# Performance work log

Measured on AMD Instinct MI355X. Metric: run time of the kernel, lower is better.

Reference implementation:

```python
import jax, jax.numpy as jnp
import numpy as np

B, T, C = 2, 2048, 1024
N_HEAD = 16
HEAD_DIM = C // N_HEAD
N_WORLDS = 4


def setup_inputs() -> dict:
    key = jax.random.key(0)
    kx, kq, kk, kv, kp, ka = jax.random.split(key, 6)
    scale = 0.02
    x = jax.random.normal(kx, (B, T, C), dtype=jnp.float32)
    Wq = jax.random.normal(kq, (C, C), dtype=jnp.float32) * scale
    Wk = jax.random.normal(kk, (C, C), dtype=jnp.float32) * scale
    Wv = jax.random.normal(kv, (C, C), dtype=jnp.float32) * scale
    Wproj = jax.random.normal(kp, (C, C), dtype=jnp.float32) * scale
    acc = jax.random.randint(ka, (N_WORLDS, N_WORLDS), 0, 2, dtype=jnp.int32)
    # ensure every world accesses itself so no softmax row is fully masked
    acc = acc.at[jnp.arange(N_WORLDS), jnp.arange(N_WORLDS)].set(1)
    return {"x": x, "Wq": Wq, "Wk": Wk, "Wv": Wv, "Wproj": Wproj,
            "accessibility": acc}


def reference(x, Wq, Wk, Wv, Wproj, accessibility):
    Bd, Td, Cd = x.shape
    # torch Linear: y = x @ W.T  -> project then split heads
    q = (x @ Wq.T).reshape(Bd, Td, N_HEAD, HEAD_DIM).transpose(0, 2, 1, 3)
    k = (x @ Wk.T).reshape(Bd, Td, N_HEAD, HEAD_DIM).transpose(0, 2, 1, 3)
    v = (x @ Wv.T).reshape(Bd, Td, N_HEAD, HEAD_DIM).transpose(0, 2, 1, 3)

    scores = jnp.einsum('bhqd,bhkd->bhqk', q, k) / jnp.sqrt(
        jnp.asarray(HEAD_DIM, dtype=x.dtype))

    # Kripke modal mask: token t lives in world t % n_worlds (necessity: \u25a1)
    world = jnp.arange(Td) % accessibility.shape[0]
    modal_mask = accessibility[world][:, world]          # (T, T) 0/1
    scores = jnp.where(modal_mask[None, None] == 0, -jnp.inf, scores)

    attn = jax.nn.softmax(scores, axis=-1)
    out = jnp.einsum('bhqk,bhkd->bhqd', attn, v)
    out = out.transpose(0, 2, 1, 3).reshape(Bd, Td, Cd)
    return out @ Wproj.T
```

## Files before the change

### kernel.cpp

```cpp
#include <hip/hip_runtime.h>
#include <hip/hip_bf16.h>
#include <stdint.h>


typedef __attribute__((ext_vector_type(8))) __bf16   bf16x8;
typedef __attribute__((ext_vector_type(4))) float    f32x4;
typedef __attribute__((ext_vector_type(8))) ushort   ushort8;

__device__ __forceinline__ ushort f2bf(float x) {
    uint32_t u = __float_as_uint(x);
    return (ushort)((u + 0x7fffu + ((u >> 16) & 1u)) >> 16);
}
__device__ __forceinline__ float sentinel(float v, float s) {
    return (fabsf(v) < 1e30f) ? v : s;
}
__device__ __forceinline__ f32x4 mfma16(bf16x8 a, bf16x8 b, f32x4 c) {
    return __builtin_amdgcn_mfma_f32_16x16x32_bf16(a, b, c, 0, 0, 0);
}
__device__ __forceinline__ ushort2 pk2(float a, float b) {
    __hip_bfloat162 h = __float22bfloat162_rn(make_float2(a, b));
    union { __hip_bfloat162 h; ushort2 u; } c; c.h = h; return c.u;
}
__device__ __forceinline__ ushort4 cvt4(float4 v) {
    ushort2 lo = pk2(v.x, v.y), hi = pk2(v.z, v.w);
    ushort4 r; r.x = lo.x; r.y = lo.y; r.z = hi.x; r.w = hi.y; return r;
}
__device__ __forceinline__ ushort4 cvt4s(float4 v, float s) {
    ushort2 lo = pk2(v.x * s, v.y * s), hi = pk2(v.z * s, v.w * s);
    ushort4 r; r.x = lo.x; r.y = lo.y; r.z = hi.x; r.w = hi.y; return r;
}
__device__ __forceinline__ float fexp2(float x) {
#if __has_builtin(__builtin_amdgcn_exp2f)
    return __builtin_amdgcn_exp2f(x);
#else
    return exp2f(x);
#endif
}
__device__ __forceinline__ void gld16(const ushort* g, ushort* l) {
    auto* g1 = reinterpret_cast<const __attribute__((address_space(1))) uint32_t*>(
        reinterpret_cast<uintptr_t>(g));
    auto* l3 = reinterpret_cast<__attribute__((address_space(3))) uint32_t*>(
        reinterpret_cast<uintptr_t>(l));
    __builtin_amdgcn_global_load_lds(g1, l3, 16, 0, 0);
}

__device__ __forceinline__ int swz(int row, int ch) {
    return row * 64 + ((ch ^ (row & 7)) * 8);
}

__device__ __forceinline__ int wperm(int ts) {
    return ((ts & 3) << 9) | (ts >> 2);
}

__device__ __forceinline__ int vshuf(int r) {
    return ((r & 31) << 2) | (r >> 5);
}

#define QSCALE 0.1803368801111244f

__global__ __launch_bounds__(256) void cvt_prepass(
        const float* __restrict__ x,  const float* __restrict__ Wq,
        const float* __restrict__ Wk, const float* __restrict__ Wv,
        const float* __restrict__ Wp,
        ushort* __restrict__ xb,  ushort* __restrict__ wqb,
        ushort* __restrict__ wkb, ushort* __restrict__ wvb,
        ushort* __restrict__ wpb)
{
    int gid = blockIdx.x;
    const float* src; ushort* dst; float sc = 1.0f; int boff;
    if (gid < 4096)      { src = x;  dst = xb;  boff = gid; }
    else if (gid < 5120) { src = Wq; dst = wqb; boff = gid - 4096; sc = QSCALE; }
    else if (gid < 6144) { src = Wk; dst = wkb; boff = gid - 5120; }
    else if (gid < 7168) { src = Wv; dst = wvb; boff = gid - 6144; }
    else                 { src = Wp; dst = wpb; boff = gid - 7168; }
    size_t idx = (size_t)boff * 1024 + threadIdx.x * 4;
    float4 v = *(const float4*)&src[idx];
    *(ushort4*)&dst[idx] = cvt4s(v, sc);
}

__global__ __launch_bounds__(256) void gemm_qkv_b(
        const ushort* __restrict__ xb,
        const ushort* __restrict__ wqb, const ushort* __restrict__ wkb,
        const ushort* __restrict__ wvb,
        ushort* __restrict__ Cq, ushort* __restrict__ Ck,
        ushort* __restrict__ Cv)
{
    __shared__ ushort As[128 * 64];
    __shared__ ushort Bs[128 * 64];

    const int lin  = blockIdx.x + 24 * blockIdx.y;
    const int xcd  = lin & 7;
    const int slot = lin >> 3;
    const int bx   = (xcd & 1) * 12 + (slot % 12);
    const int by   = (xcd >> 1) * 8 + (slot / 12);

    const int sel = bx >> 3;
    const ushort* __restrict__ Bw = sel == 0 ? wqb : (sel == 1 ? wkb : wvb);
    ushort* __restrict__ C        = sel == 0 ? Cq : (sel == 1 ? Ck : Cv);

    const int tid  = threadIdx.x;
    const int lane = tid & 63;
    const int wave = tid >> 6;
    const int quad = lane >> 4;
    const int l15  = lane & 15;
    const int tokb = by * 128;
    const int chb  = (bx & 7) * 128;
    const int wm = (wave & 1) * 64, wn = (wave >> 1) * 64;

    f32x4 acc[4][4] = {};

    for (int k0 = 0; k0 < 1024; k0 += 64) {
        __syncthreads();
        #pragma unroll
        for (int j = 0; j < 4; ++j) {
            int cb = j * 256 + wave * 64;
            int ci = cb + lane;
            int r  = ci >> 3;
            int qc = (ci & 7) ^ (r & 7);
            if (sel < 2) {
                gld16(&Bw[(size_t)(chb + r) * 1024 + k0 + qc * 8], &As[cb * 8]);
                gld16(&xb[(size_t)(tokb + r) * 1024 + k0 + qc * 8], &Bs[cb * 8]);
            } else {
                gld16(&xb[(size_t)(tokb + vshuf(r)) * 1024 + k0 + qc * 8], &As[cb * 8]);
                gld16(&Bw[(size_t)(chb + r) * 1024 + k0 + qc * 8], &Bs[cb * 8]);
            }
        }
        __syncthreads();

        bf16x8 af[2][4], bfr[2][4];
        #pragma unroll
        for (int f = 0; f < 2; ++f)
            #pragma unroll
            for (int i = 0; i < 4; ++i) {
                int ch = f * 4 + quad;
                af[f][i]  = *(const bf16x8*)&As[swz(wm + i * 16 + l15, ch)];
                bfr[f][i] = *(const bf16x8*)&Bs[swz(wn + i * 16 + l15, ch)];
            }
        #pragma unroll
        for (int f = 0; f < 2; ++f)
            #pragma unroll
            for (int i = 0; i < 4; ++i)
                #pragma unroll
                for (int t = 0; t < 4; ++t)
                    acc[i][t] = mfma16(af[f][i], bfr[f][t], acc[i][t]);
    }

    if (sel < 2) {
        #pragma unroll
        for (int i = 0; i < 4; ++i) {
            int ch = chb + wm + i * 16 + quad * 4;
            int hh = ch >> 6, d0 = ch & 63;
            #pragma unroll
            for (int t = 0; t < 4; ++t) {
                int n = tokb + wn + t * 16 + l15;
                int b = n >> 11, ts = n & 2047;
                ushort4 hv;
                hv.x = f2bf(sentinel(acc[i][t][0], 1e8f));
                hv.y = f2bf(sentinel(acc[i][t][1], 1e8f));
                hv.z = f2bf(sentinel(acc[i][t][2], 1e8f));
                hv.w = f2bf(sentinel(acc[i][t][3], 1e8f));
                *(ushort4*)&C[((size_t)((b << 4) | hh) * 2048 + wperm(ts)) * 64 + d0] = hv;
            }
        }
    } else {
        const int b = tokb >> 11;
        #pragma unroll
        for (int i = 0; i < 4; ++i) {
            int mi0 = wm + i * 16 + quad * 4;
            int colbase = ((mi0 >> 5) << 9) + ((tokb & 2047) >> 2) + (mi0 & 31);
            #pragma unroll
            for (int t = 0; t < 4; ++t) {
                int n = chb + wn + t * 16 + l15;
                int hh = n >> 6, d = n & 63;
                ushort4 hv;
                hv.x = f2bf(sentinel(acc[i][t][0], 1e8f));
                hv.y = f2bf(sentinel(acc[i][t][1], 1e8f));
                hv.z = f2bf(sentinel(acc[i][t][2], 1e8f));
                hv.w = f2bf(sentinel(acc[i][t][3], 1e8f));
                *(ushort4*)&C[((size_t)((b << 4) | hh) * 64 + d) * 2048 + colbase] = hv;
            }
        }
    }
}

__global__ __launch_bounds__(256) void gemm_proj_b(
        const ushort* __restrict__ O, const ushort* __restrict__ wpb,
        float* __restrict__ out)
{
    __shared__ ushort As[128 * 64];
    __shared__ ushort Bs[64 * 64];

    const int lin  = blockIdx.x + 16 * blockIdx.y;
    const int xcd  = lin & 7;
    const int slot = lin >> 3;
    const int bx   = (xcd & 1) * 8 + (slot % 8);
    const int by   = (xcd >> 1) * 8 + (slot / 8);

    const int tid  = threadIdx.x;
    const int lane = tid & 63;
    const int wave = tid >> 6;
    const int quad = lane >> 4;
    const int l15  = lane & 15;
    const int bm = by * 128, bn = bx * 64;
    const int wm = (wave & 1) * 64,  wn = (wave >> 1) * 32;

    f32x4 acc[4][2] = {};

    for (int k0 = 0; k0 < 1024; k0 += 64) {
        __syncthreads();
        int h = k0 >> 6;
        #pragma unroll
        for (int j = 0; j < 4; ++j) {
            int cb = j * 256 + wave * 64;
            int ci = cb + lane;
            int r  = ci >> 3;
            int qc = (ci & 7) ^ (r & 7);
            int m = bm + r;
            int b = m >> 11, ts = m & 2047;
            gld16(&O[((((size_t)(b * 16 + h)) * 2048 + wperm(ts)) << 6) + qc * 8],
                  &As[cb * 8]);
        }
        #pragma unroll
        for (int j = 0; j < 2; ++j) {
            int cb = j * 256 + wave * 64;
            int ci = cb + lane;
            int r  = ci >> 3;
            int qc = (ci & 7) ^ (r & 7);
            gld16(&wpb[(size_t)(bn + r) * 1024 + k0 + qc * 8], &Bs[cb * 8]);
        }
        __syncthreads();

        bf16x8 af[2][4], bfr[2][2];
        #pragma unroll
        for (int f = 0; f < 2; ++f) {
            int ch = f * 4 + quad;
            #pragma unroll
            for (int i = 0; i < 4; ++i)
                af[f][i] = *(const bf16x8*)&As[swz(wm + i * 16 + l15, ch)];
            #pragma unroll
            for (int t = 0; t < 2; ++t)
                bfr[f][t] = *(const bf16x8*)&Bs[swz(wn + t * 16 + l15, ch)];
        }
        #pragma unroll
        for (int f = 0; f < 2; ++f)
            #pragma unroll
            for (int i = 0; i < 4; ++i)
                #pragma unroll
                for (int t = 0; t < 2; ++t)
                    acc[i][t] = mfma16(af[f][i], bfr[f][t], acc[i][t]);
    }

    #pragma unroll
    for (int i = 0; i < 4; ++i)
        #pragma unroll
        for (int t = 0; t < 2; ++t)
            #pragma unroll
            for (int r = 0; r < 4; ++r) {
                int m = bm + wm + i * 16 + quad * 4 + r;
                int n = bn + wn + t * 16 + l15;
                out[(size_t)m * 1024 + n] = sentinel(acc[i][t][r], 100.0f);
            }
}

__global__ __launch_bounds__(256) void attn_kernel(
        ushort* __restrict__ Q, const ushort* __restrict__ Kk,
        const ushort* __restrict__ Vt_g, const int* __restrict__ accm)
{
    __shared__ ushort Ks[2][64 * 64];
    __shared__ ushort Vt[2][64 * 64];
    __shared__ ushort Ps[4][32 * 64];

    const int tid  = threadIdx.x;
    const int lane = tid & 63;
    const int wave = tid >> 6;
    const int quad = lane >> 4;
    const int l15  = lane & 15;
    const int bh = blockIdx.x, qt = blockIdx.y;

    ushort*       Qg = Q    + ((size_t)bh * 2048 + qt * 128) * 64;
    const ushort* Kg = Kk   + (size_t)bh * 2048 * 64;
    const ushort* Vg = Vt_g + (size_t)bh * 64 * 2048;

    const int qworld = qt >> 2;
    int gpack = 0, ng = 0;
    #pragma unroll
    for (int w = 0; w < 4; ++w)
        if (accm[qworld * 4 + w] != 0) { gpack |= w << (ng * 8); ++ng; }
    const int nkt = ng * 8;
    auto ktof = [&](int i) {
        return ((((gpack >> ((i >> 3) << 3)) & 3) << 3) | (i & 7));
    };

    bf16x8 aq[2][2];
    #pragma unroll
    for (int i = 0; i < 2; ++i)
        #pragma unroll
        for (int f = 0; f < 2; ++f)
            aq[i][f] = *(const bf16x8*)
                &Qg[(wave * 32 + i * 16 + l15) * 64 + f * 32 + quad * 8];

    bf16x8 aones;
    #pragma unroll
    for (int j = 0; j < 8; ++j) aones[j] = (__bf16)1.0f;

    f32x4 oacc[4][2] = {};
    f32x4 lacc[2] = {};

    auto stage = [&](int kt, int buf) {
        #pragma unroll
        for (int j = 0; j < 2; ++j) {
            int cb = j * 256 + wave * 64;
            int ci = cb + lane;
            int r  = ci >> 3;
            int qc = (ci & 7) ^ (r & 7);
            gld16(&Kg[((size_t)kt * 64 + r) * 64 + qc * 8], &Ks[buf][cb * 8]);
            gld16(&Vg[(size_t)r * 2048 + kt * 64 + qc * 8], &Vt[buf][cb * 8]);
        }
    };

    stage(ktof(0), 0);
    for (int it = 0; it < nkt; ++it) {
        const int cur = it & 1;
        __syncthreads();
        if (it < nkt - 1) stage(ktof(it + 1), cur ^ 1);

        f32x4 st[4][2] = {};
        #pragma unroll
        for (int f = 0; f < 2; ++f) {
            int ch = f * 4 + quad;
            #pragma unroll
            for (int k4 = 0; k4 < 4; ++k4) {
                bf16x8 ak = *(const bf16x8*)&Ks[cur][swz(k4 * 16 + l15, ch)];
                #pragma unroll
                for (int i = 0; i < 2; ++i)
                    st[k4][i] = mfma16(ak, aq[i][f], st[k4][i]);
            }
        }

        #pragma unroll
        for (int i = 0; i < 2; ++i) {
            int prow = i * 16 + l15;
            #pragma unroll
            for (int k4 = 0; k4 < 4; ++k4) {
                float p0 = fexp2(st[k4][i][0]);
                float p1 = fexp2(st[k4][i][1]);
                float p2 = fexp2(st[k4][i][2]);
                float p3 = fexp2(st[k4][i][3]);
                ushort2 lo = pk2(p0, p1), hi = pk2(p2, p3);
                ushort4 pv4; pv4.x = lo.x; pv4.y = lo.y;
                pv4.z = hi.x; pv4.w = hi.y;
                int pc8 = (k4 * 2 + (quad >> 1)) ^ (l15 & 7);
                *(ushort4*)&Ps[wave][prow * 64 + pc8 * 8 + (quad & 1) * 4] = pv4;
            }
        }

        bf16x8 bp[2][2];
        #pragma unroll
        for (int i = 0; i < 2; ++i)
            #pragma unroll
            for (int f = 0; f < 2; ++f)
                bp[i][f] = *(const bf16x8*)&Ps[wave][swz(i * 16 + l15, f * 4 + quad)];
        #pragma unroll
        for (int f = 0; f < 2; ++f) {
            int ch = f * 4 + quad;
            #pragma unroll
            for (int i = 0; i < 2; ++i)
                lacc[i] = mfma16(aones, bp[i][f], lacc[i]);
            #pragma unroll
            for (int dt = 0; dt < 4; ++dt) {
                bf16x8 av = *(const bf16x8*)&Vt[cur][swz(dt * 16 + l15, ch)];
                #pragma unroll
                for (int i = 0; i < 2; ++i)
                    oacc[dt][i] = mfma16(av, bp[i][f], oacc[dt][i]);
            }
        }
    }

    #pragma unroll
    for (int i = 0; i < 2; ++i) {
        const float inv = 1.0f / lacc[i][0];
        #pragma unroll
        for (int dt = 0; dt < 4; ++dt) {
            ushort4 o4;
            o4.x = f2bf(sentinel(oacc[dt][i][0] * inv, 1e4f));
            o4.y = f2bf(sentinel(oacc[dt][i][1] * inv, 1e4f));
            o4.z = f2bf(sentinel(oacc[dt][i][2] * inv, 1e4f));
            o4.w = f2bf(sentinel(oacc[dt][i][3] * inv, 1e4f));
            *(ushort4*)&Qg[(wave * 32 + i * 16 + l15) * 64 + dt * 16 + quad * 4] = o4;
        }
    }
}

__global__ __launch_bounds__(256) void gemm_qkv_f32(
        const float* __restrict__ A,
        const float* __restrict__ Wq, const float* __restrict__ Wk,
        const float* __restrict__ Wv,
        ushort* __restrict__ Cq, ushort* __restrict__ Ck,
        ushort* __restrict__ Cv)
{
    __shared__ __align__(16) ushort As[128 * 72];
    __shared__ __align__(16) ushort Bs[128 * 72];

    const int sel = blockIdx.x >> 3;
    const float* __restrict__ Bw = sel == 0 ? Wq : (sel == 1 ? Wk : Wv);
    ushort* __restrict__ C       = sel == 0 ? Cq : (sel == 1 ? Ck : Cv);
    const float scale = sel == 0 ? QSCALE : 1.0f;

    const int tid  = threadIdx.x;
    const int lane = tid & 63;
    const int wave = tid >> 6;
    const int quad = lane >> 4;
    const int l15  = lane & 15;
    const int bm = blockIdx.y * 128;
    const int bn = (blockIdx.x & 7) * 128;
    const int wm = (wave & 1) * 64, wn = (wave >> 1) * 64;

    f32x4 acc[4][4] = {};

    for (int k0 = 0; k0 < 1024; k0 += 64) {
        __syncthreads();
        #pragma unroll
        for (int i = 0; i < 8; ++i) {
            int c = tid + 256 * i;
            int row = c >> 4, col = (c & 15) * 4;
            int rg = (sel == 2) ? vshuf(row) : row;
            float4 a4 = *(const float4*)&A[(size_t)(bm + rg) * 1024 + k0 + col];
            *(ushort4*)&As[row * 72 + col] = cvt4(a4);
            float4 b4 = *(const float4*)&Bw[(size_t)(bn + row) * 1024 + k0 + col];
            *(ushort4*)&Bs[row * 72 + col] = cvt4s(b4, scale);
        }
        __syncthreads();

        bf16x8 af[2][4], bfr[2][4];
        #pragma unroll
        for (int f = 0; f < 2; ++f)
            #pragma unroll
            for (int i = 0; i < 4; ++i) {
                af[f][i]  = *(const bf16x8*)&As[(wm + i * 16 + l15) * 72 + f * 32 + quad * 8];
                bfr[f][i] = *(const bf16x8*)&Bs[(wn + i * 16 + l15) * 72 + f * 32 + quad * 8];
            }
        #pragma unroll
        for (int f = 0; f < 2; ++f)
            #pragma unroll
            for (int i = 0; i < 4; ++i)
                #pragma unroll
                for (int t = 0; t < 4; ++t)
                    acc[i][t] = mfma16(af[f][i], bfr[f][t], acc[i][t]);
    }

    if (sel < 2) {
        #pragma unroll
        for (int i = 0; i < 4; ++i)
            #pragma unroll
            for (int t = 0; t < 4; ++t)
                #pragma unroll
                for (int r = 0; r < 4; ++r) {
                    int m = bm + wm + i * 16 + quad * 4 + r;
                    int n = bn + wn + t * 16 + l15;
                    int b = m >> 11, ts = m & 2047, hh = n >> 6, d = n & 63;
                    C[((size_t)((b << 4) | hh) * 2048 + wperm(ts)) * 64 + d] =
                        f2bf(sentinel(acc[i][t][r], 1e8f));
                }
    } else {
        const int b = bm >> 11;
        #pragma unroll
        for (int i = 0; i < 4; ++i) {
            int mi0 = wm + i * 16 + quad * 4;
            int colbase = ((mi0 >> 5) << 9) + ((bm & 2047) >> 2) + (mi0 & 31);
            #pragma unroll
            for (int t = 0; t < 4; ++t) {
                int n = bn + wn + t * 16 + l15;
                int hh = n >> 6, d = n & 63;
                ushort4 hv;
                hv.x = f2bf(sentinel(acc[i][t][0], 1e8f));
                hv.y = f2bf(sentinel(acc[i][t][1], 1e8f));
                hv.z = f2bf(sentinel(acc[i][t][2], 1e8f));
                hv.w = f2bf(sentinel(acc[i][t][3], 1e8f));
                *(ushort4*)&C[((size_t)((b << 4) | hh) * 64 + d) * 2048 + colbase] = hv;
            }
        }
    }
}

__global__ __launch_bounds__(256) void gemm_proj_f32(
        const ushort* __restrict__ A, const float* __restrict__ Bw,
        float* __restrict__ C)
{
    __shared__ __align__(16) ushort As[128 * 72];
    __shared__ __align__(16) ushort Bs[64 * 72];

    const int tid  = threadIdx.x;
    const int lane = tid & 63;
    const int wave = tid >> 6;
    const int quad = lane >> 4;
    const int l15  = lane & 15;
    const int bm = blockIdx.y * 128, bn = blockIdx.x * 64;
    const int wm = (wave & 1) * 64,  wn = (wave >> 1) * 32;

    f32x4 acc[4][2] = {};

    for (int k0 = 0; k0 < 1024; k0 += 64) {
        __syncthreads();
        #pragma unroll
        for (int i = 0; i < 4; ++i) {
            int c = tid + 256 * i;
            int row = c >> 3, col = (c & 7) * 8;
            int m = bm + row;
            int b = m >> 11, ts = m & 2047, h = k0 >> 6;
            size_t aoff = ((((size_t)(b * 16 + h)) * 2048 + wperm(ts)) << 6) + col;
            *(ushort8*)&As[row * 72 + col] = *(const ushort8*)&A[aoff];
        }
        #pragma unroll
        for (int i = 0; i < 4; ++i) {
            int c = tid + 256 * i;
            int row = c >> 4, col = (c & 15) * 4;
            float4 b4 = *(const float4*)&Bw[(size_t)(bn + row) * 1024 + k0 + col];
            *(ushort4*)&Bs[row * 72 + col] = cvt4(b4);
        }
        __syncthreads();

        bf16x8 af[2][4], bfr[2][2];
        #pragma unroll
        for (int f = 0; f < 2; ++f) {
            #pragma unroll
            for (int i = 0; i < 4; ++i)
                af[f][i] = *(const bf16x8*)&As[(wm + i * 16 + l15) * 72 + f * 32 + quad * 8];
            #pragma unroll
            for (int t = 0; t < 2; ++t)
                bfr[f][t] = *(const bf16x8*)&Bs[(wn + t * 16 + l15) * 72 + f * 32 + quad * 8];
        }
        #pragma unroll
        for (int f = 0; f < 2; ++f)
            #pragma unroll
            for (int i = 0; i < 4; ++i)
                #pragma unroll
                for (int t = 0; t < 2; ++t)
                    acc[i][t] = mfma16(af[f][i], bfr[f][t], acc[i][t]);
    }

    #pragma unroll
    for (int i = 0; i < 4; ++i)
        #pragma unroll
        for (int t = 0; t < 2; ++t)
            #pragma unroll
            for (int r = 0; r < 4; ++r) {
                int m = bm + wm + i * 16 + quad * 4 + r;
                int n = bn + wn + t * 16 + l15;
                C[(size_t)m * 1024 + n] = sentinel(acc[i][t][r], 100.0f);
            }
}

__global__ void diag_kernel(float* out, int n, float val) {
    int i = blockIdx.x * blockDim.x + threadIdx.x;
    if (i < n) out[i] = (i == 0) ? val : 0.f;
}

extern "C" void kernel_launch(void* const* d_in, const int* in_sizes, int n_in,
                              void* d_out, int out_size, void* d_ws, size_t ws_size,
                              hipStream_t stream) {
    const float* x  = (const float*)d_in[0];
    const float* Wq = (const float*)d_in[1];
    const float* Wk = (const float*)d_in[2];
    const float* Wv = (const float*)d_in[3];
    const float* Wp = (const float*)d_in[4];
    const int* accm = (const int*)d_in[5];
    float* out = (float*)d_out;

    const size_t SZ = (size_t)4 * 1024 * 1024;
    const size_t WSZ = (size_t)1024 * 1024;

    if (ws_size < 3 * SZ * sizeof(ushort)) {
        diag_kernel<<<(out_size + 255) / 256, 256, 0, stream>>>(
            out, out_size, (float)ws_size);
        return;
    }

    ushort* k_ws = (ushort*)d_ws;
    ushort* v_ws = k_ws + SZ;
    ushort* q_ws = v_ws + SZ;
    dim3 blk(256);

    const size_t need_fast = (4 * SZ + 4 * WSZ) * sizeof(ushort);
    if (ws_size >= need_fast) {
        ushort* xb  = q_ws + SZ;
        ushort* wqb = xb + SZ;
        ushort* wkb = wqb + WSZ;
        ushort* wvb = wkb + WSZ;
        ushort* wpb = wvb + WSZ;
        cvt_prepass<<<8192, blk, 0, stream>>>(x, Wq, Wk, Wv, Wp,
                                              xb, wqb, wkb, wvb, wpb);
        gemm_qkv_b<<<dim3(24, 32), blk, 0, stream>>>(xb, wqb, wkb, wvb,
                                                     q_ws, k_ws, v_ws);
        attn_kernel<<<dim3(32, 16), blk, 0, stream>>>(q_ws, k_ws, v_ws, accm);
        gemm_proj_b<<<dim3(16, 32), blk, 0, stream>>>(q_ws, wpb, out);
    } else {
        gemm_qkv_f32<<<dim3(24, 32), blk, 0, stream>>>(x, Wq, Wk, Wv,
                                                       q_ws, k_ws, v_ws);
        attn_kernel<<<dim3(32, 16), blk, 0, stream>>>(q_ws, k_ws, v_ws, accm);
        gemm_proj_f32<<<dim3(16, 32), blk, 0, stream>>>(q_ws, Wp, out);
    }
}
```

Baseline: 159.2 us.

## Retile QKV GEMM to 256x256 blocks with double-buffered LDS and 512 threads

The QKV projection GEMM moves from 128x128 tiles with 256 threads and a single LDS buffer to 256x256 tiles with 512 threads (8 waves) and a K-step of 32. LDS is double-buffered so the next slice's global-to-LDS copy is issued before the current slice is computed, which removes one barrier per step. The grid drops from 768 to 192 blocks, and the V-path row shuffle and output index math are adjusted to the new tile size. Each wave holds more accumulators (8x4 MFMA tiles), which raises register pressure. With only 192 blocks the GPU's compute units may not all be kept busy.

```diff
diff --git a/kernel.cpp b/kernel.cpp
--- a/kernel.cpp
+++ b/kernel.cpp
@@ -54,6 +54,9 @@
 
 __device__ __forceinline__ int vshuf(int r) {
     return ((r & 31) << 2) | (r >> 5);
+}
+__device__ __forceinline__ int vshufX(int r) {
+    return ((r & 63) << 2) | (r >> 6);
 }
 
 #define QSCALE 0.1803368801111244f
@@ -78,105 +81,122 @@
     *(ushort4*)&dst[idx] = cvt4s(v, sc);
 }
 
-__global__ __launch_bounds__(256) void gemm_qkv_b(
+__global__ __launch_bounds__(512, 2) void gemm_qkv_b(
         const ushort* __restrict__ xb,
         const ushort* __restrict__ wqb, const ushort* __restrict__ wkb,
         const ushort* __restrict__ wvb,
         ushort* __restrict__ Cq, ushort* __restrict__ Ck,
         ushort* __restrict__ Cv)
 {
-    __shared__ ushort As[128 * 64];
-    __shared__ ushort Bs[128 * 64];
-
-    const int lin  = blockIdx.x + 24 * blockIdx.y;
-    const int xcd  = lin & 7;
-    const int slot = lin >> 3;
-    const int bx   = (xcd & 1) * 12 + (slot % 12);
-    const int by   = (xcd >> 1) * 8 + (slot / 12);
-
-    const int sel = bx >> 3;
-    const ushort* __restrict__ Bw = sel == 0 ? wqb : (sel == 1 ? wkb : wvb);
-    ushort* __restrict__ C        = sel == 0 ? Cq : (sel == 1 ? Ck : Cv);
+    __shared__ ushort As[2][256 * 32];
+    __shared__ ushort Bs[2][256 * 32];
 
     const int tid  = threadIdx.x;
     const int lane = tid & 63;
     const int wave = tid >> 6;
     const int quad = lane >> 4;
     const int l15  = lane & 15;
-    const int tokb = by * 128;
-    const int chb  = (bx & 7) * 128;
-    const int wm = (wave & 1) * 64, wn = (wave >> 1) * 64;
-
-    f32x4 acc[4][4] = {};
-
-    for (int k0 = 0; k0 < 1024; k0 += 64) {
-        __syncthreads();
-        #pragma unroll
-        for (int j = 0; j < 4; ++j) {
-            int cb = j * 256 + wave * 64;
-            int ci = cb + lane;
-            int r  = ci >> 3;
-            int qc = (ci & 7) ^ (r & 7);
-            if (sel < 2) {
-                gld16(&Bw[(size_t)(chb + r) * 1024 + k0 + qc * 8], &As[cb * 8]);
-                gld16(&xb[(size_t)(tokb + r) * 1024 + k0 + qc * 8], &Bs[cb * 8]);
-            } else {
-                gld16(&xb[(size_t)(tokb + vshuf(r)) * 1024 + k0 + qc * 8], &As[cb * 8]);
-                gld16(&Bw[(size_t)(chb + r) * 1024 + k0 + qc * 8], &Bs[cb * 8]);
-            }
-        }
-        __syncthreads();
-
-        bf16x8 af[2][4], bfr[2][4];
-        #pragma unroll
-        for (int f = 0; f < 2; ++f)
-            #pragma unroll
-            for (int i = 0; i < 4; ++i) {
-                int ch = f * 4 + quad;
-                af[f][i]  = *(const bf16x8*)&As[swz(wm + i * 16 + l15, ch)];
-                bfr[f][i] = *(const bf16x8*)&Bs[swz(wn + i * 16 + l15, ch)];
-            }
-        #pragma unroll
-        for (int f = 0; f < 2; ++f)
-            #pragma unroll
-            for (int i = 0; i < 4; ++i)
-                #pragma unroll
-                for (int t = 0; t < 4; ++t)
-                    acc[i][t] = mfma16(af[f][i], bfr[f][t], acc[i][t]);
-    }
-
-    if (sel < 2) {
-        #pragma unroll
-        for (int i = 0; i < 4; ++i) {
-            int ch = chb + wm + i * 16 + quad * 4;
+    const int wm2  = wave >> 2;
+    const int wn4  = wave & 3;
+
+    const int bid = blockIdx.x;
+    const bool isV = bid >= 128;
+    int tokb, chO;
+    const ushort* __restrict__ Aw;
+    ushort* __restrict__ C;
+    if (!isV) {
+        const int blkM = bid & 7;
+        const int blkN = bid >> 3;
+        tokb = blkN * 256;
+        const int chb2 = blkM * 256;
+        chO  = chb2 & 1023;
+        Aw = (blkM < 4) ? (wqb + (size_t)chb2 * 1024)
+                        : (wkb + (size_t)(chb2 - 1024) * 1024);
+        C  = (blkM < 4) ? Cq : Ck;
+    } else {
+        const int v = bid - 128;
+        tokb = (v & 15) * 256;
+        chO  = (v >> 4) * 256;
+        Aw = wvb + (size_t)chO * 1024;
+        C  = Cv;
+    }
+
+    auto stage = [&](int kt, int buf) {
+        const int kcol = kt * 32;
+        #pragma unroll
+        for (int j = 0; j < 2; ++j) {
+            int ci = j * 512 + tid;
+            int r  = ci >> 2;
+            int qc = (((ci & 3) ^ (r & 3) ^ ((r >> 2) & 3))) * 8;
+            const ushort* asrc = isV ? &xb[(size_t)(tokb + vshufX(r)) * 1024]
+                                     : &Aw[(size_t)r * 1024];
+            const ushort* bsrc = isV ? &Aw[(size_t)r * 1024]
+                                     : &xb[(size_t)(tokb + r) * 1024];
+            gld16(&asrc[kcol + qc], &As[buf][ci * 8]);
+            gld16(&bsrc[kcol + qc], &Bs[buf][ci * 8]);
+        }
+    };
+
+    f32x4 acc[8][4] = {};
+
+    stage(0, 0);
+    for (int t = 0; t < 32; ++t) {
+        const int cur = t & 1;
+        __syncthreads();
+        if (t < 31) stage(t + 1, cur ^ 1);
+
+        bf16x8 af[8], bf[4];
+        #pragma unroll
+        for (int i = 0; i < 8; ++i) {
+            int row = wm2 * 128 + i * 16 + l15;
+            int pos = quad ^ (row & 3) ^ ((row >> 2) & 3);
+            af[i] = *(const bf16x8*)&As[cur][row * 32 + pos * 8];
+        }
+        #pragma unroll
+        for (int tt = 0; tt < 4; ++tt) {
+            int row = wn4 * 64 + tt * 16 + l15;
+            int pos = quad ^ (row & 3) ^ ((row >> 2) & 3);
+            bf[tt] = *(const bf16x8*)&Bs[cur][row * 32 + pos * 8];
+        }
+        #pragma unroll
+        for (int i = 0; i < 8; ++i)
+            #pragma unroll
+            for (int tt = 0; tt < 4; ++tt)
+                acc[i][tt] = mfma16(af[i], bf[tt], acc[i][tt]);
+    }
+
+    if (!isV) {
+        #pragma unroll
+        for (int i = 0; i < 8; ++i) {
+            int ch = chO + wm2 * 128 + i * 16 + quad * 4;
             int hh = ch >> 6, d0 = ch & 63;
             #pragma unroll
-            for (int t = 0; t < 4; ++t) {
-                int n = tokb + wn + t * 16 + l15;
+            for (int tt = 0; tt < 4; ++tt) {
+                int n = tokb + wn4 * 64 + tt * 16 + l15;
                 int b = n >> 11, ts = n & 2047;
                 ushort4 hv;
-                hv.x = f2bf(sentinel(acc[i][t][0], 1e8f));
-                hv.y = f2bf(sentinel(acc[i][t][1], 1e8f));
-                hv.z = f2bf(sentinel(acc[i][t][2], 1e8f));
-                hv.w = f2bf(sentinel(acc[i][t][3], 1e8f));
+                hv.x = f2bf(sentinel(acc[i][tt][0], 1e8f));
+                hv.y = f2bf(sentinel(acc[i][tt][1], 1e8f));
+                hv.z = f2bf(sentinel(acc[i][tt][2], 1e8f));
+                hv.w = f2bf(sentinel(acc[i][tt][3], 1e8f));
                 *(ushort4*)&C[((size_t)((b << 4) | hh) * 2048 + wperm(ts)) * 64 + d0] = hv;
             }
         }
     } else {
         const int b = tokb >> 11;
         #pragma unroll
-        for (int i = 0; i < 4; ++i) {
-            int mi0 = wm + i * 16 + quad * 4;
-            int colbase = ((mi0 >> 5) << 9) + ((tokb & 2047) >> 2) + (mi0 & 31);
-            #pragma unroll
-            for (int t = 0; t < 4; ++t) {
-                int n = chb + wn + t * 16 + l15;
+        for (int i = 0; i < 8; ++i) {
+            int mi0 = wm2 * 128 + i * 16 + quad * 4;
+            int colbase = ((mi0 >> 6) << 9) + ((tokb & 2047) >> 2) + (mi0 & 63);
+            #pragma unroll
+            for (int tt = 0; tt < 4; ++tt) {
+                int n = chO + wn4 * 64 + tt * 16 + l15;
                 int hh = n >> 6, d = n & 63;
                 ushort4 hv;
-                hv.x = f2bf(sentinel(acc[i][t][0], 1e8f));
-                hv.y = f2bf(sentinel(acc[i][t][1], 1e8f));
-                hv.z = f2bf(sentinel(acc[i][t][2], 1e8f));
-                hv.w = f2bf(sentinel(acc[i][t][3], 1e8f));
+                hv.x = f2bf(sentinel(acc[i][tt][0], 1e8f));
+                hv.y = f2bf(sentinel(acc[i][tt][1], 1e8f));
+                hv.z = f2bf(sentinel(acc[i][tt][2], 1e8f));
+                hv.w = f2bf(sentinel(acc[i][tt][3], 1e8f));
                 *(ushort4*)&C[((size_t)((b << 4) | hh) * 64 + d) * 2048 + colbase] = hv;
             }
         }
@@ -589,8 +609,8 @@
         ushort* wpb = wvb + WSZ;
         cvt_prepass<<<8192, blk, 0, stream>>>(x, Wq, Wk, Wv, Wp,
                                               xb, wqb, wkb, wvb, wpb);
-        gemm_qkv_b<<<dim3(24, 32), blk, 0, stream>>>(xb, wqb, wkb, wvb,
-                                                     q_ws, k_ws, v_ws);
+        gemm_qkv_b<<<dim3(192), dim3(512), 0, stream>>>(xb, wqb, wkb, wvb,
+                                                        q_ws, k_ws, v_ws);
         attn_kernel<<<dim3(32, 16), blk, 0, stream>>>(q_ws, k_ws, v_ws, accm);
         gemm_proj_b<<<dim3(16, 32), blk, 0, stream>>>(q_ws, wpb, out);
     } else {
```

Result: slower. 163.6 us (+2.8%).
